# Performance work log

Hardware: AMD Instinct MI355X
Metric: run time of the kernel (lower is better)

The kernel has to match this reference:

```python
import jax, jax.numpy as jnp
import numpy as np

POOLED_H = 7
POOLED_W = 7
SPATIAL_SCALE = 0.0625
B, C, H, W = 8, 256, 48, 48
R = 300
IMG = 768  # = H / SPATIAL_SCALE


def setup_inputs() -> dict:
    key = jax.random.key(0)
    k1, k2, k3, k4 = jax.random.split(key, 4)
    features = jax.random.normal(k1, (B, C, H, W), dtype=jnp.float32)
    # rois: (batch_idx, x1, y1, x2, y2) in input-image coords
    bidx = jax.random.randint(k2, (R, 1), 0, B).astype(jnp.float32)
    tl = jax.random.uniform(k3, (R, 2), minval=0.0, maxval=IMG - 64.0)
    wh = jax.random.uniform(k4, (R, 2), minval=32.0, maxval=320.0)
    br = jnp.minimum(tl + wh, IMG - 1.0)
    rois = jnp.concatenate([bidx, tl, br], axis=1).astype(jnp.float32)
    return {"features": features, "rois": rois}


def _hat_integral(x, grid):
    """Integral from -inf to x of the unit hat basis function centered at each
    grid point g (support [g-1, g+1], peak 1, total mass 1).
    x: [..., 1-broadcastable], grid: [G] -> returns [..., G]."""
    t = x[..., None] - (grid - 1.0)
    return jnp.where(
        t <= 0.0, 0.0,
        jnp.where(t <= 1.0, 0.5 * t * t,
                  jnp.where(t <= 2.0, 1.0 - 0.5 * (2.0 - t) ** 2, 1.0)))


def reference(features, rois):
    # Precise RoI Pooling: exact double integral of the bilinear interpolant
    # over each bin, divided by bin area. Bilinear interp (with zero padding
    # outside the map, as in the CUDA PrRoIPoolingGetData) is
    #   f(u,v) = sum_{j,i} feat[j,i] * hat_j(v) * hat_i(u)
    # so the bin integral factorizes into per-axis hat-integral weights.
    Bf, Cf, Hf, Wf = features.shape
    bidx = rois[:, 0].astype(jnp.int32)
    x1 = rois[:, 1] * SPATIAL_SCALE
    y1 = rois[:, 2] * SPATIAL_SCALE
    x2 = rois[:, 3] * SPATIAL_SCALE
    y2 = rois[:, 4] * SPATIAL_SCALE
    roi_w = jnp.maximum(x2 - x1, 0.0)
    roi_h = jnp.maximum(y2 - y1, 0.0)
    bin_w = roi_w / POOLED_W  # [R]
    bin_h = roi_h / POOLED_H

    ph = jnp.arange(POOLED_H, dtype=jnp.float32)
    pw = jnp.arange(POOLED_W, dtype=jnp.float32)
    ya = y1[:, None] + ph[None, :] * bin_h[:, None]  # [R, PH]
    yb = ya + bin_h[:, None]
    xa = x1[:, None] + pw[None, :] * bin_w[:, None]  # [R, PW]
    xb = xa + bin_w[:, None]

    gy = jnp.arange(Hf, dtype=jnp.float32)
    gx = jnp.arange(Wf, dtype=jnp.float32)
    Wy = _hat_integral(yb, gy) - _hat_integral(ya, gy)  # [R, PH, H]
    Wx = _hat_integral(xb, gx) - _hat_integral(xa, gx)  # [R, PW, W]

    feat = features[bidx]  # [R, C, H, W]
    t = jnp.einsum('rpj,rcji->rcpi', Wy, feat)   # integrate over y
    num = jnp.einsum('rqi,rcpi->rcpq', Wx, t)    # integrate over x -> [R,C,PH,PW]

    area = (bin_w * bin_h)[:, None, None, None]  # win_size per ROI
    out = jnp.where(area > 0.0, num / jnp.where(area > 0.0, area, 1.0), 0.0)
    return out
```

## Files before the change

kernel.cpp:

```cpp
#include <hip/hip_runtime.h>


#define PH 7
#define PW 7
#define NBINS 49
#define SCALE 0.0625f
#define CH 256
#define FH 48
#define FW 48
#define RNUM 300
#define PRM 128
#define PATCHF (23 * 56)
#define RSF 328

__device__ __forceinline__ float hat_int(float x, float g) {
    float t = x - (g - 1.0f);
    if (t <= 0.0f) return 0.0f;
    if (t <= 1.0f) return 0.5f * t * t;
    if (t <= 2.0f) { float u = 2.0f - t; return 1.0f - 0.5f * u * u; }
    return 1.0f;
}

__global__ __launch_bounds__(256)
void prroi_prep(const float* __restrict__ rois, float* __restrict__ prm) {
    const int r = blockIdx.x * 4 + (threadIdx.x >> 6);
    const int t = threadIdx.x & 63;
    if (r >= RNUM || t >= 15) return;

    const float* roi = rois + r * 5;
    const int   b  = (int)roi[0];
    const float x1 = roi[1] * SCALE, y1 = roi[2] * SCALE;
    const float x2 = roi[3] * SCALE, y2 = roi[4] * SCALE;
    const float roi_w = fmaxf(x2 - x1, 0.0f), roi_h = fmaxf(y2 - y1, 0.0f);
    const float bin_w = roi_w / (float)PW, bin_h = roi_h / (float)PH;
    const float area = bin_w * bin_h;
    const float inv_area = (area > 0.0f) ? (1.0f / area) : 0.0f;

    const float ylo = fminf(y1, y2), yhi = fmaxf(y1, y2);
    const float xlo = fminf(x1, x2), xhi = fmaxf(x1, x2);
    const int j1 = min(FH - 1, (int)floorf(yhi) + 1);
    const int i1 = min(FW - 1, (int)floorf(xhi) + 1);
    const int J0 = min(max(0, (int)floorf(ylo) - 1), FH - 6);
    const int I0 = min(max(0, (int)floorf(xlo) - 1) & ~3, FW - 8);
    const int JROWS = min(FH - J0, max(j1 - J0 + 1, 6));
    int NI4 = min(((i1 - I0) >> 2) + 1, (FW - I0) >> 2);
    NI4 = max(NI4, 2);

    float* p = prm + (size_t)r * PRM;
    if (t < PH) {
        const int ph = t;
        const float ya = y1 + ph * bin_h, yb = ya + bin_h;
        const int base = min(max((int)floorf(ya) - 1, J0), J0 + JROWS - 6);
        p[ph * 8 + 6] = __int_as_float(base - J0);
#pragma unroll
        for (int k = 0; k < 6; ++k) {
            const float g = (float)(base + k);
            p[ph * 8 + k] = hat_int(yb, g) - hat_int(ya, g);
        }
    } else if (t < PH + PW) {
        const int pw = t - PH;
        const float xa = x1 + pw * bin_w, xb = xa + bin_w;
        const int base = min(max((int)floorf(xa) - 1, I0), I0 + 4 * NI4 - 6);
        p[56 + pw * 8 + 6] = __int_as_float(base - I0);
#pragma unroll
        for (int k = 0; k < 6; ++k) {
            const float g = (float)(base + k);
            p[56 + pw * 8 + k] = hat_int(xb, g) - hat_int(xa, g);
        }
    } else {
        p[112] = inv_area;
        p[113] = __int_as_float(b);
        p[114] = __int_as_float(J0);
        p[115] = __int_as_float(I0);
        p[116] = __int_as_float(JROWS);
        p[117] = __int_as_float(NI4);
    }
}

__global__ __launch_bounds__(256, 6)
void prroi_main(const float* __restrict__ feat,
                const float* __restrict__ prm,
                float* __restrict__ out) {
    const int wv   = threadIdx.x >> 6;
    const int lane = threadIdx.x & 63;
    const int r    = blockIdx.y;
    const int c4   = blockIdx.x * 4 + wv;
    const int c0   = c4 * 4;

    __shared__ float lds[4][PATCHF + RSF];
    float* patch = lds[wv];
    float* rsw   = lds[wv] + PATCHF;

    const float* p = prm + (size_t)r * PRM;
    const float4 h0 = *(const float4*)(p + 112);
    const float2 h1 = *(const float2*)(p + 116);
    const float ia  = h0.x;
    const int b     = __float_as_int(h0.y);
    const int J0    = __float_as_int(h0.z);
    const int I0    = __float_as_int(h0.w);
    const int JROWS = __float_as_int(h1.x);
    const int NI4   = __float_as_int(h1.y);

    const int  pwA = lane >> 3, jsl = lane & 7;
    const bool actA = lane < 56;
    float wx0 = 0, wx1 = 0, wx2 = 0, wx3 = 0, wx4 = 0, wx5 = 0;
    int biA = 0;
    if (actA) {
        const float4 wa = *(const float4*)(p + 56 + pwA * 8);
        const float4 wb = *(const float4*)(p + 56 + pwA * 8 + 4);
        wx0 = wa.x; wx1 = wa.y; wx2 = wa.z; wx3 = wa.w;
        wx4 = wb.x; wx5 = wb.y; biA = __float_as_int(wb.z);
    }
    const bool actB = lane < NBINS;
    float wy0 = 0, wy1 = 0, wy2 = 0, wy3 = 0, wy4 = 0, wy5 = 0;
    int pwB = 0, bjB = 0;
    if (actB) {
        const int ph = lane / 7;
        pwB = lane - ph * 7;
        const float4 ua = *(const float4*)(p + ph * 8);
        const float4 ub = *(const float4*)(p + ph * 8 + 4);
        wy0 = ua.x; wy1 = ua.y; wy2 = ua.z; wy3 = ua.w;
        wy4 = ub.x; wy5 = ub.y; bjB = __float_as_int(ub.z);
    }

    const int NU = JROWS << 3;
    const float* fb = feat + (size_t)(b * CH + c0) * (FH * FW);
    const float* srcp[3];
    bool act_[3]; int dst_[3];
    float4 pa0[3], pa1[3], pb0[3], pb1[3];
#pragma unroll
    for (int s = 0; s < 3; ++s) {
        const int u  = lane + (s << 6);
        const int j  = u >> 3, i4 = u & 7;
        const bool a = (u < NU) && (i4 < NI4);
        act_[s] = a;
        dst_[s] = j * 56 + 8 * i4;
        srcp[s] = fb + (size_t)(J0 + j) * FW + I0 + 4 * i4;
        if (a) {
            pa0[s] = *(const float4*)(srcp[s]);
            pa1[s] = *(const float4*)(srcp[s] + FH * FW);
        }
    }
#pragma unroll
    for (int s = 0; s < 3; ++s) {
        if (act_[s]) {
            pb0[s] = *(const float4*)(srcp[s] + 2 * FH * FW);
            pb1[s] = *(const float4*)(srcp[s] + 3 * FH * FW);
        }
    }

#pragma unroll
    for (int s = 0; s < 3; ++s) {
        if (act_[s]) {
            float* d = patch + dst_[s];
            *(float4*)(d + 0) = make_float4(pa0[s].x, pa1[s].x, pa0[s].y, pa1[s].y);
            *(float4*)(d + 4) = make_float4(pa0[s].z, pa1[s].z, pa0[s].w, pa1[s].w);
        }
    }
    asm volatile("s_waitcnt lgkmcnt(0)" ::: "memory");

#pragma unroll 1
    for (int it = 0; it < 2; ++it) {
        if (actA) {
            for (int jr = jsl; jr < JROWS; jr += 8) {
                const float* row = patch + jr * 56 + 2 * biA;
                const float2 v0 = *(const float2*)(row + 0);
                const float2 v1 = *(const float2*)(row + 2);
                const float2 v2 = *(const float2*)(row + 4);
                const float2 v3 = *(const float2*)(row + 6);
                const float2 v4 = *(const float2*)(row + 8);
                const float2 v5 = *(const float2*)(row + 10);
                float ax = 0.0f, ay = 0.0f;
                ax += wx0 * v0.x; ay += wx0 * v0.y;
                ax += wx1 * v1.x; ay += wx1 * v1.y;
                ax += wx2 * v2.x; ay += wx2 * v2.y;
                ax += wx3 * v3.x; ay += wx3 * v3.y;
                ax += wx4 * v4.x; ay += wx4 * v4.y;
                ax += wx5 * v5.x; ay += wx5 * v5.y;
                *(float2*)&rsw[(pwA * 23 + jr) * 2] = make_float2(ax, ay);
            }
        }
        asm volatile("s_waitcnt lgkmcnt(0)" ::: "memory");

        if (actB) {
            const float* rb = rsw + (pwB * 23 + bjB) * 2;
            const float2 u0 = *(const float2*)(rb + 0);
            const float2 u1 = *(const float2*)(rb + 2);
            const float2 u2 = *(const float2*)(rb + 4);
            const float2 u3 = *(const float2*)(rb + 6);
            const float2 u4 = *(const float2*)(rb + 8);
            const float2 u5 = *(const float2*)(rb + 10);
            float ax = 0.0f, ay = 0.0f;
            ax += wy0 * u0.x; ay += wy0 * u0.y;
            ax += wy1 * u1.x; ay += wy1 * u1.y;
            ax += wy2 * u2.x; ay += wy2 * u2.y;
            ax += wy3 * u3.x; ay += wy3 * u3.y;
            ax += wy4 * u4.x; ay += wy4 * u4.y;
            ax += wy5 * u5.x; ay += wy5 * u5.y;
            float* o = out + ((size_t)r * CH + c0 + 2 * it) * NBINS + lane;
            o[0]     = ax * ia;
            o[NBINS] = ay * ia;
        }

        if (it == 0) {
            asm volatile("s_waitcnt lgkmcnt(0)" ::: "memory");
#pragma unroll
            for (int s = 0; s < 3; ++s) {
                if (act_[s]) {
                    float* d = patch + dst_[s];
                    *(float4*)(d + 0) = make_float4(pb0[s].x, pb1[s].x, pb0[s].y, pb1[s].y);
                    *(float4*)(d + 4) = make_float4(pb0[s].z, pb1[s].z, pb0[s].w, pb1[s].w);
                }
            }
            asm volatile("s_waitcnt lgkmcnt(0)" ::: "memory");
        }
    }
}

extern "C" void kernel_launch(void* const* d_in, const int* in_sizes, int n_in,
                              void* d_out, int out_size, void* d_ws, size_t ws_size,
                              hipStream_t stream) {
    const float* feat = (const float*)d_in[0];
    const float* rois = (const float*)d_in[1];
    float* out = (float*)d_out;
    float* prm = (float*)d_ws;

    prroi_prep<<<(RNUM + 3) / 4, 256, 0, stream>>>(rois, prm);
    prroi_main<<<dim3(16, RNUM), 256, 0, stream>>>(feat, prm, out);
}
```

Baseline: 87.15 us.

## Fuse ROI prep into main kernel and halve channels per wave

```diff
diff --git a/kernel.cpp b/kernel.cpp
--- a/kernel.cpp
+++ b/kernel.cpp
@@ -9,7 +9,6 @@
 #define FH 48
 #define FW 48
 #define RNUM 300
-#define PRM 128
 #define PATCHF (23 * 56)
 #define RSF 328
 
@@ -21,20 +20,29 @@
     return 1.0f;
 }
 
-__global__ __launch_bounds__(256)
-void prroi_prep(const float* __restrict__ rois, float* __restrict__ prm) {
-    const int r = blockIdx.x * 4 + (threadIdx.x >> 6);
-    const int t = threadIdx.x & 63;
-    if (r >= RNUM || t >= 15) return;
+__global__ __launch_bounds__(256, 6)
+void prroi_one(const float* __restrict__ feat,
+               const float* __restrict__ rois,
+               float* __restrict__ out) {
+    const int wv   = threadIdx.x >> 6;
+    const int lane = threadIdx.x & 63;
+    const int r    = blockIdx.y;
+    const int cpr  = blockIdx.x * 4 + wv;
+    const int c0   = cpr * 2;
+
+    __shared__ float lds[4][PATCHF + RSF];
+    float* patch = lds[wv];
+    float* rsw   = lds[wv] + PATCHF;
 
     const float* roi = rois + r * 5;
-    const int   b  = (int)roi[0];
-    const float x1 = roi[1] * SCALE, y1 = roi[2] * SCALE;
-    const float x2 = roi[3] * SCALE, y2 = roi[4] * SCALE;
+    const float f0 = roi[0], f1 = roi[1], f2 = roi[2], f3 = roi[3], f4 = roi[4];
+    const int   b  = (int)f0;
+    const float x1 = f1 * SCALE, y1 = f2 * SCALE;
+    const float x2 = f3 * SCALE, y2 = f4 * SCALE;
     const float roi_w = fmaxf(x2 - x1, 0.0f), roi_h = fmaxf(y2 - y1, 0.0f);
     const float bin_w = roi_w / (float)PW, bin_h = roi_h / (float)PH;
     const float area = bin_w * bin_h;
-    const float inv_area = (area > 0.0f) ? (1.0f / area) : 0.0f;
+    const float ia   = (area > 0.0f) ? (1.0f / area) : 0.0f;
 
     const float ylo = fminf(y1, y2), yhi = fmaxf(y1, y2);
     const float xlo = fminf(x1, x2), xhi = fmaxf(x1, x2);
@@ -46,70 +54,38 @@
     int NI4 = min(((i1 - I0) >> 2) + 1, (FW - I0) >> 2);
     NI4 = max(NI4, 2);
 
-    float* p = prm + (size_t)r * PRM;
-    if (t < PH) {
-        const int ph = t;
-        const float ya = y1 + ph * bin_h, yb = ya + bin_h;
-        const int base = min(max((int)floorf(ya) - 1, J0), J0 + JROWS - 6);
-        p[ph * 8 + 6] = __int_as_float(base - J0);
+    const int NU = JROWS << 3;
+    const float* fb = feat + (size_t)(b * CH + c0) * (FH * FW);
+    bool act_[3]; int dst_[3];
+    float4 pc0[3], pc1[3];
 #pragma unroll
-        for (int k = 0; k < 6; ++k) {
-            const float g = (float)(base + k);
-            p[ph * 8 + k] = hat_int(yb, g) - hat_int(ya, g);
+    for (int s = 0; s < 3; ++s) {
+        const int u  = lane + (s << 6);
+        const int j  = u >> 3, i4 = u & 7;
+        const bool a = (u < NU) && (i4 < NI4);
+        act_[s] = a;
+        dst_[s] = j * 56 + 8 * i4;
+        if (a) {
+            const float* src = fb + (size_t)(J0 + j) * FW + I0 + 4 * i4;
+            pc0[s] = *(const float4*)(src);
+            pc1[s] = *(const float4*)(src + FH * FW);
         }
-    } else if (t < PH + PW) {
-        const int pw = t - PH;
-        const float xa = x1 + pw * bin_w, xb = xa + bin_w;
-        const int base = min(max((int)floorf(xa) - 1, I0), I0 + 4 * NI4 - 6);
-        p[56 + pw * 8 + 6] = __int_as_float(base - I0);
-#pragma unroll
-        for (int k = 0; k < 6; ++k) {
-            const float g = (float)(base + k);
-            p[56 + pw * 8 + k] = hat_int(xb, g) - hat_int(xa, g);
-        }
-    } else {
-        p[112] = inv_area;
-        p[113] = __int_as_float(b);
-        p[114] = __int_as_float(J0);
-        p[115] = __int_as_float(I0);
-        p[116] = __int_as_float(JROWS);
-        p[117] = __int_as_float(NI4);
     }
-}
-
-__global__ __launch_bounds__(256, 6)
-void prroi_main(const float* __restrict__ feat,
-                const float* __restrict__ prm,
-                float* __restrict__ out) {
-    const int wv   = threadIdx.x >> 6;
-    const int lane = threadIdx.x & 63;
-    const int r    = blockIdx.y;
-    const int c4   = blockIdx.x * 4 + wv;
-    const int c0   = c4 * 4;
-
-    __shared__ float lds[4][PATCHF + RSF];
-    float* patch = lds[wv];
-    float* rsw   = lds[wv] + PATCHF;
-
-    const float* p = prm + (size_t)r * PRM;
-    const float4 h0 = *(const float4*)(p + 112);
-    const float2 h1 = *(const float2*)(p + 116);
-    const float ia  = h0.x;
-    const int b     = __float_as_int(h0.y);
-    const int J0    = __float_as_int(h0.z);
-    const int I0    = __float_as_int(h0.w);
-    const int JROWS = __float_as_int(h1.x);
-    const int NI4   = __float_as_int(h1.y);
 
     const int  pwA = lane >> 3, jsl = lane & 7;
     const bool actA = lane < 56;
     float wx0 = 0, wx1 = 0, wx2 = 0, wx3 = 0, wx4 = 0, wx5 = 0;
     int biA = 0;
     if (actA) {
-        const float4 wa = *(const float4*)(p + 56 + pwA * 8);
-        const float4 wb = *(const float4*)(p + 56 + pwA * 8 + 4);
-        wx0 = wa.x; wx1 = wa.y; wx2 = wa.z; wx3 = wa.w;
-        wx4 = wb.x; wx5 = wb.y; biA = __float_as_int(wb.z);
+        const float xa = x1 + pwA * bin_w, xb = xa + bin_w;
+        const int base = min(max((int)floorf(xa) - 1, I0), I0 + 4 * NI4 - 6);
+        biA = base - I0;
+        wx0 = hat_int(xb, (float)(base + 0)) - hat_int(xa, (float)(base + 0));
+        wx1 = hat_int(xb, (float)(base + 1)) - hat_int(xa, (float)(base + 1));
+        wx2 = hat_int(xb, (float)(base + 2)) - hat_int(xa, (float)(base + 2));
+        wx3 = hat_int(xb, (float)(base + 3)) - hat_int(xa, (float)(base + 3));
+        wx4 = hat_int(xb, (float)(base + 4)) - hat_int(xa, (float)(base + 4));
+        wx5 = hat_int(xb, (float)(base + 5)) - hat_int(xa, (float)(base + 5));
     }
     const bool actB = lane < NBINS;
     float wy0 = 0, wy1 = 0, wy2 = 0, wy3 = 0, wy4 = 0, wy5 = 0;
@@ -117,103 +93,66 @@
     if (actB) {
         const int ph = lane / 7;
         pwB = lane - ph * 7;
-        const float4 ua = *(const float4*)(p + ph * 8);
-        const float4 ub = *(const float4*)(p + ph * 8 + 4);
-        wy0 = ua.x; wy1 = ua.y; wy2 = ua.z; wy3 = ua.w;
-        wy4 = ub.x; wy5 = ub.y; bjB = __float_as_int(ub.z);
-    }
-
-    const int NU = JROWS << 3;
-    const float* fb = feat + (size_t)(b * CH + c0) * (FH * FW);
-    const float* srcp[3];
-    bool act_[3]; int dst_[3];
-    float4 pa0[3], pa1[3], pb0[3], pb1[3];
-#pragma unroll
-    for (int s = 0; s < 3; ++s) {
-        const int u  = lane + (s << 6);
-        const int j  = u >> 3, i4 = u & 7;
-        const bool a = (u < NU) && (i4 < NI4);
-        act_[s] = a;
-        dst_[s] = j * 56 + 8 * i4;
-        srcp[s] = fb + (size_t)(J0 + j) * FW + I0 + 4 * i4;
-        if (a) {
-            pa0[s] = *(const float4*)(srcp[s]);
-            pa1[s] = *(const float4*)(srcp[s] + FH * FW);
-        }
-    }
-#pragma unroll
-    for (int s = 0; s < 3; ++s) {
-        if (act_[s]) {
-            pb0[s] = *(const float4*)(srcp[s] + 2 * FH * FW);
-            pb1[s] = *(const float4*)(srcp[s] + 3 * FH * FW);
-        }
+        const float ya = y1 + ph * bin_h, yb = ya + bin_h;
+        const int base = min(max((int)floorf(ya) - 1, J0), J0 + JROWS - 6);
+        bjB = base - J0;
+        wy0 = hat_int(yb, (float)(base + 0)) - hat_int(ya, (float)(base + 0));
+        wy1 = hat_int(yb, (float)(base + 1)) - hat_int(ya, (float)(base + 1));
+        wy2 = hat_int(yb, (float)(base + 2)) - hat_int(ya, (float)(base + 2));
+        wy3 = hat_int(yb, (float)(base + 3)) - hat_int(ya, (float)(base + 3));
+        wy4 = hat_int(yb, (float)(base + 4)) - hat_int(ya, (float)(base + 4));
+        wy5 = hat_int(yb, (float)(base + 5)) - hat_int(ya, (float)(base + 5));
     }
 
 #pragma unroll
     for (int s = 0; s < 3; ++s) {
         if (act_[s]) {
             float* d = patch + dst_[s];
-            *(float4*)(d + 0) = make_float4(pa0[s].x, pa1[s].x, pa0[s].y, pa1[s].y);
-            *(float4*)(d + 4) = make_float4(pa0[s].z, pa1[s].z, pa0[s].w, pa1[s].w);
+            *(float4*)(d + 0) = make_float4(pc0[s].x, pc1[s].x, pc0[s].y, pc1[s].y);
+            *(float4*)(d + 4) = make_float4(pc0[s].z, pc1[s].z, pc0[s].w, pc1[s].w);
         }
     }
     asm volatile("s_waitcnt lgkmcnt(0)" ::: "memory");
 
-#pragma unroll 1
-    for (int it = 0; it < 2; ++it) {
-        if (actA) {
-            for (int jr = jsl; jr < JROWS; jr += 8) {
-                const float* row = patch + jr * 56 + 2 * biA;
-                const float2 v0 = *(const float2*)(row + 0);
-                const float2 v1 = *(const float2*)(row + 2);
-                const float2 v2 = *(const float2*)(row + 4);
-                const float2 v3 = *(const float2*)(row + 6);
-                const float2 v4 = *(const float2*)(row + 8);
-                const float2 v5 = *(const float2*)(row + 10);
-                float ax = 0.0f, ay = 0.0f;
-                ax += wx0 * v0.x; ay += wx0 * v0.y;
-                ax += wx1 * v1.x; ay += wx1 * v1.y;
-                ax += wx2 * v2.x; ay += wx2 * v2.y;
-                ax += wx3 * v3.x; ay += wx3 * v3.y;
-                ax += wx4 * v4.x; ay += wx4 * v4.y;
-                ax += wx5 * v5.x; ay += wx5 * v5.y;
-                *(float2*)&rsw[(pwA * 23 + jr) * 2] = make_float2(ax, ay);
-            }
+    if (actA) {
+        for (int jr = jsl; jr < JROWS; jr += 8) {
+            const float* row = patch + jr * 56 + 2 * biA;
+            const float2 v0 = *(const float2*)(row + 0);
+            const float2 v1 = *(const float2*)(row + 2);
+            const float2 v2 = *(const float2*)(row + 4);
+            const float2 v3 = *(const float2*)(row + 6);
+            const float2 v4 = *(const float2*)(row + 8);
+            const float2 v5 = *(const float2*)(row + 10);
+            float ax = 0.0f, ay = 0.0f;
+            ax += wx0 * v0.x; ay += wx0 * v0.y;
+            ax += wx1 * v1.x; ay += wx1 * v1.y;
+            ax += wx2 * v2.x; ay += wx2 * v2.y;
+            ax += wx3 * v3.x; ay += wx3 * v3.y;
+            ax += wx4 * v4.x; ay += wx4 * v4.y;
+            ax += wx5 * v5.x; ay += wx5 * v5.y;
+            *(float2*)&rsw[(pwA * 23 + jr) * 2] = make_float2(ax, ay);
         }
-        asm volatile("s_waitcnt lgkmcnt(0)" ::: "memory");
+    }
+    asm volatile("s_waitcnt lgkmcnt(0)" ::: "memory");
 
-        if (actB) {
-            const float* rb = rsw + (pwB * 23 + bjB) * 2;
-            const float2 u0 = *(const float2*)(rb + 0);
-            const float2 u1 = *(const float2*)(rb + 2);
-            const float2 u2 = *(const float2*)(rb + 4);
-            const float2 u3 = *(const float2*)(rb + 6);
-            const float2 u4 = *(const float2*)(rb + 8);
-            const float2 u5 = *(const float2*)(rb + 10);
-            float ax = 0.0f, ay = 0.0f;
-            ax += wy0 * u0.x; ay += wy0 * u0.y;
-            ax += wy1 * u1.x; ay += wy1 * u1.y;
-            ax += wy2 * u2.x; ay += wy2 * u2.y;
-            ax += wy3 * u3.x; ay += wy3 * u3.y;
-            ax += wy4 * u4.x; ay += wy4 * u4.y;
-            ax += wy5 * u5.x; ay += wy5 * u5.y;
-            float* o = out + ((size_t)r * CH + c0 + 2 * it) * NBINS + lane;
-            o[0]     = ax * ia;
-            o[NBINS] = ay * ia;
-        }
-
-        if (it == 0) {
-            asm volatile("s_waitcnt lgkmcnt(0)" ::: "memory");
-#pragma unroll
-            for (int s = 0; s < 3; ++s) {
-                if (act_[s]) {
-                    float* d = patch + dst_[s];
-                    *(float4*)(d + 0) = make_float4(pb0[s].x, pb1[s].x, pb0[s].y, pb1[s].y);
-                    *(float4*)(d + 4) = make_float4(pb0[s].z, pb1[s].z, pb0[s].w, pb1[s].w);
-                }
-            }
-            asm volatile("s_waitcnt lgkmcnt(0)" ::: "memory");
-        }
+    if (actB) {
+        const float* rb = rsw + (pwB * 23 + bjB) * 2;
+        const float2 u0 = *(const float2*)(rb + 0);
+        const float2 u1 = *(const float2*)(rb + 2);
+        const float2 u2 = *(const float2*)(rb + 4);
+        const float2 u3 = *(const float2*)(rb + 6);
+        const float2 u4 = *(const float2*)(rb + 8);
+        const float2 u5 = *(const float2*)(rb + 10);
+        float ax = 0.0f, ay = 0.0f;
+        ax += wy0 * u0.x; ay += wy0 * u0.y;
+        ax += wy1 * u1.x; ay += wy1 * u1.y;
+        ax += wy2 * u2.x; ay += wy2 * u2.y;
+        ax += wy3 * u3.x; ay += wy3 * u3.y;
+        ax += wy4 * u4.x; ay += wy4 * u4.y;
+        ax += wy5 * u5.x; ay += wy5 * u5.y;
+        float* o = out + ((size_t)r * CH + c0) * NBINS + lane;
+        o[0]     = ax * ia;
+        o[NBINS] = ay * ia;
     }
 }
 
@@ -223,8 +162,7 @@
     const float* feat = (const float*)d_in[0];
     const float* rois = (const float*)d_in[1];
     float* out = (float*)d_out;
-    float* prm = (float*)d_ws;
+    (void)d_ws; (void)ws_size;
 
-    prroi_prep<<<(RNUM + 3) / 4, 256, 0, stream>>>(rois, prm);
-    prroi_main<<<dim3(16, RNUM), 256, 0, stream>>>(feat, prm, out);
+    prroi_one<<<dim3(32, RNUM), 256, 0, stream>>>(feat, rois, out);
 }
```

Result: slower. 88.93 us (+2.0%).
